# Kernel tuning notes

Measured on AMD Instinct MI355X. Metric: run time of the kernel, lower is better.

The kernel has to match this reference:

```python
import jax, jax.numpy as jnp
import numpy as np

N_NODES = 100000


def gcn_conv(x, edge_index, W, b):
    """PyG-style GCNConv: self-loops + symmetric norm + scatter-add aggregation."""
    n = x.shape[0]
    loop = jnp.arange(n, dtype=edge_index.dtype)
    src = jnp.concatenate([edge_index[0], loop])  # [E+N]
    dst = jnp.concatenate([edge_index[1], loop])  # [E+N]
    # degree of target nodes (edge weight = 1)
    deg = jax.ops.segment_sum(jnp.ones_like(dst, dtype=x.dtype), dst, num_segments=n)
    dinv = jnp.where(deg > 0, jax.lax.rsqrt(deg), 0.0)
    norm = dinv[src] * dinv[dst]  # [E+N]
    h = x @ W                      # [N, out] linear (bias added post-aggregation)
    msg = h[src] * norm[:, None]   # [E+N, out]
    out = jax.ops.segment_sum(msg, dst, num_segments=n)
    return out + b


def setup_inputs() -> dict:
    key = jax.random.key(0)
    ks = jax.random.split(key, 8)
    n, e = N_NODES, 3200000
    x = jax.random.normal(ks[0], (n, 11), dtype=jnp.float32)
    edge_index = jax.random.randint(ks[1], (2, e), 0, n, dtype=jnp.int32)
    def glorot(k, fi, fo):
        s = jnp.sqrt(6.0 / (fi + fo))
        return jax.random.uniform(k, (fi, fo), dtype=jnp.float32, minval=-s, maxval=s)
    return {
        "x": x,
        "edge_index": edge_index,
        "W1": glorot(ks[2], 11, 16), "b1": jnp.zeros((16,), jnp.float32),
        "W2": glorot(ks[3], 16, 32), "b2": jnp.zeros((32,), jnp.float32),
        "W3": glorot(ks[4], 32, 64), "b3": jnp.zeros((64,), jnp.float32),
    }


def reference(x, edge_index, W1, b1, W2, b2, W3, b3):
    # dropout is identity in eval mode
    h = jax.nn.relu(gcn_conv(x, edge_index, W1, b1))
    h = jax.nn.relu(gcn_conv(h, edge_index, W2, b2))
    return gcn_conv(h, edge_index, W3, b3)
```

## Files before the change

### kernel.cpp

```cpp
#include <hip/hip_runtime.h>
#include <hip/hip_fp16.h>

#define NPB_SHIFT 7
#define NPB       128
#define CHUNK     8192
#define STAGE_CAP 8192
#define NBKT_MAX  1024

union U2H { unsigned u; __half2 h; };

__device__ inline float2 h2f(unsigned u) {
    U2H c; c.u = u;
    return __half22float2(c.h);
}

__device__ inline unsigned f2h(float a, float b) {
    U2H c; c.h = __float22half2_rn(make_float2(a, b));
    return c.u;
}


__global__ void hist_kernel(const int* __restrict__ dst, int* __restrict__ hist,
                            int E, int HBr, int nbkt) {
    __shared__ int bins[NBKT_MAX];
    int tid = threadIdx.x;
    for (int i = tid; i < nbkt; i += 512) bins[i] = 0;
    __syncthreads();
    int start = blockIdx.x * CHUNK;
    #pragma unroll
    for (int j = 0; j < 16; ++j) {
        int e = start + j * 512 + tid;
        if (e < E) atomicAdd(&bins[dst[e] >> NPB_SHIFT], 1);
    }
    __syncthreads();
    for (int i = tid; i < nbkt; i += 512)
        hist[(size_t)i * HBr + blockIdx.x] = bins[i];
}


__global__ void scan_block8_kernel(int* data, int* __restrict__ partial, int len) {
    __shared__ int wtot[16];
    int tid = threadIdx.x, lane = tid & 63, wid = tid >> 6;
    int base = blockIdx.x * 8192 + tid * 8;
    int v[8]; int s = 0;
    #pragma unroll
    for (int j = 0; j < 8; ++j) {
        int i = base + j;
        v[j] = (i < len) ? data[i] : 0;
        s += v[j];
    }
    int inc = s;
    #pragma unroll
    for (int o = 1; o < 64; o <<= 1) { int t = __shfl_up(inc, o); if (lane >= o) inc += t; }
    if (lane == 63) wtot[wid] = inc;
    __syncthreads();
    if (tid == 0) {
        int run = 0;
        #pragma unroll
        for (int w = 0; w < 16; ++w) { int t = wtot[w]; wtot[w] = run; run += t; }
        partial[blockIdx.x] = run;
    }
    __syncthreads();
    int excl = wtot[wid] + inc - s;
    #pragma unroll
    for (int j = 0; j < 8; ++j) {
        int i = base + j;
        if (i < len) data[i] = excl;
        excl += v[j];
    }
}

__global__ void scan_partials_kernel(int* partial, int nb) {
    int t = threadIdx.x;
    int i0 = 2 * t, i1 = 2 * t + 1;
    int v0 = (i0 < nb) ? partial[i0] : 0;
    int v1 = (i1 < nb) ? partial[i1] : 0;
    int s = v0 + v1;
    int inc = s;
    #pragma unroll
    for (int o = 1; o < 64; o <<= 1) { int u = __shfl_up(inc, o); if (t >= o) inc += u; }
    int excl = inc - s;
    if (i0 < nb) partial[i0] = excl;
    if (i1 < nb) partial[i1] = excl + v0;
}


__global__ void scatter_kernel(const int* __restrict__ src, const int* __restrict__ dst,
                               const int* __restrict__ offbuf, const int* __restrict__ partial,
                               int* __restrict__ ebuf, int E, int HBr, int nbkt) {
    __shared__ int gbase[NBKT_MAX];
    __shared__ int thist[NBKT_MAX];
    __shared__ int toff[NBKT_MAX + 1];
    __shared__ int stage[CHUNK];
    __shared__ unsigned short bstage[CHUNK];
    __shared__ int wtot8[8];
    int tid = threadIdx.x, lane = tid & 63, wid = tid >> 6;
    for (int i = tid; i < nbkt; i += 512) {
        size_t idx = (size_t)i * HBr + blockIdx.x;
        gbase[i] = offbuf[idx] + partial[(int)(idx >> 13)];
    }
    for (int i = tid; i < NBKT_MAX; i += 512) thist[i] = 0;
    __syncthreads();
    int start = blockIdx.x * CHUNK;
    int s_[16], d_[16], r_[16];
    #pragma unroll
    for (int j = 0; j < 16; ++j) {
        int e = start + j * 512 + tid;
        if (e < E) {
            s_[j] = src[e];
            d_[j] = dst[e];
            r_[j] = atomicAdd(&thist[d_[j] >> NPB_SHIFT], 1);
        } else {
            d_[j] = -1;
        }
    }
    __syncthreads();
    int a0 = thist[2 * tid], a1 = thist[2 * tid + 1];
    int ss = a0 + a1;
    int inc = ss;
    #pragma unroll
    for (int o = 1; o < 64; o <<= 1) { int t = __shfl_up(inc, o); if (lane >= o) inc += t; }
    if (lane == 63) wtot8[wid] = inc;
    __syncthreads();
    int wbase = 0;
    for (int w = 0; w < wid; ++w) wbase += wtot8[w];
    int excl = wbase + inc - ss;
    toff[2 * tid]     = excl;
    toff[2 * tid + 1] = excl + a0;
    if (tid == 511) toff[1024] = excl + ss;
    __syncthreads();
    #pragma unroll
    for (int j = 0; j < 16; ++j) {
        if (d_[j] >= 0) {
            int b = d_[j] >> NPB_SHIFT;
            int q = toff[b] + r_[j];
            stage[q]  = ((d_[j] & (NPB - 1)) << 17) | s_[j];
            bstage[q] = (unsigned short)b;
        }
    }
    __syncthreads();
    int total = toff[1024];
    for (int j = tid; j < total; j += 512) {
        int b = bstage[j];
        ebuf[gbase[b] + (j - toff[b])] = stage[j];
    }
}


__global__ void bucket_build_kernel(const int* __restrict__ ebuf, const int* __restrict__ offbuf,
                                    const int* __restrict__ partial, const float* __restrict__ x,
                                    int* __restrict__ csr_src, int* __restrict__ row_start,
                                    float* __restrict__ dinv, unsigned* __restrict__ g0h,
                                    int E, int HBr, int nbkt, int n) {
    __shared__ int cnt[NPB], cur[NPB];
    __shared__ float dnl[NPB];
    __shared__ int stage[STAGE_CAP];
    __shared__ int wtot2[2];
    int tid = threadIdx.x;
    int k = blockIdx.x;
    size_t ib = (size_t)k * HBr;
    int bb = offbuf[ib] + partial[(int)(ib >> 13)];
    int be;
    if (k + 1 < nbkt) {
        size_t ie = (size_t)(k + 1) * HBr;
        be = offbuf[ie] + partial[(int)(ie >> 13)];
    } else be = E;
    int bsize = be - bb;
    if (tid < NPB) cnt[tid] = 0;
    __syncthreads();

    constexpr int J = 20;
    int v[J], r[J];
    bool fast = (bsize <= J * 256) && (bsize <= STAGE_CAP);
    if (fast) {
        #pragma unroll
        for (int j = 0; j < J; ++j) {
            int e = bb + tid + j * 256;
            if (e < be) { v[j] = ebuf[e]; r[j] = atomicAdd(&cnt[v[j] >> 17], 1); }
            else v[j] = -1;
        }
    } else {
        for (int e = bb + tid; e < be; e += 256) atomicAdd(&cnt[ebuf[e] >> 17], 1);
    }
    __syncthreads();

    int lane = tid & 63, wid = tid >> 6;
    int c = 0, inc = 0;
    if (tid < NPB) {
        c = cnt[tid];
        inc = c;
        #pragma unroll
        for (int o = 1; o < 64; o <<= 1) { int t = __shfl_up(inc, o); if (lane >= o) inc += t; }
        if (lane == 63) wtot2[wid] = inc;
    }
    __syncthreads();
    if (tid < NPB) {
        int base = (wid == 1) ? wtot2[0] : 0;
        int excl = base + inc - c;
        cur[tid] = excl;
        int node = k * NPB + tid;
        if (node < n) {
            row_start[node] = bb + excl;
            float dn = rsqrtf((float)(c + 1));
            dinv[node] = dn;
            dnl[tid] = dn;
        }
    }
    if (k == 0 && tid == 0) row_start[n] = E;
    __syncthreads();

    {
        int base_node = k * NPB;
        for (int i = tid; i < NPB * 8; i += 256) {
            int ln = i >> 3, kk = i & 7;
            int node = base_node + ln;
            if (node < n) {
                float dn = dnl[ln];
                int f0 = 2 * kk, f1 = f0 + 1;
                float a = (f0 < 11) ? x[(size_t)node * 11 + f0] * dn : 0.f;
                float b = (f1 < 11) ? x[(size_t)node * 11 + f1] * dn : 0.f;
                g0h[(size_t)node * 8 + kk] = f2h(a, b);
            }
        }
    }

    if (fast) {
        #pragma unroll
        for (int j = 0; j < J; ++j)
            if (v[j] >= 0) stage[cur[v[j] >> 17] + r[j]] = v[j] & 0x1FFFF;
        __syncthreads();
        for (int j = tid; j < bsize; j += 256) csr_src[bb + j] = stage[j];
    } else if (bsize <= STAGE_CAP) {
        for (int e = bb + tid; e < be; e += 256) {
            int vv = ebuf[e];
            int rr = atomicAdd(&cur[vv >> 17], 1);
            stage[rr] = vv & 0x1FFFF;
        }
        __syncthreads();
        for (int j = tid; j < bsize; j += 256) csr_src[bb + j] = stage[j];
    } else {
        for (int e = bb + tid; e < be; e += 256) {
            int vv = ebuf[e];
            int rr = atomicAdd(&cur[vv >> 17], 1);
            csr_src[bb + rr] = vv & 0x1FFFF;
        }
    }
}


template <int LPR, int NB>
__device__ inline void gather_batch_h(const uint2* __restrict__ gv, const int* __restrict__ csr,
                                      int p, int end, int nrem, int q, int grp, float* acc) {
    constexpr int NGRP = 16 / LPR;
    int s[NB]; float m[NB];
    #pragma unroll
    for (int u = 0; u < NB; ++u) {
        int slot = u * NGRP + grp;
        s[u] = csr[min(p + slot, end - 1)];
        m[u] = (slot < nrem) ? 1.f : 0.f;
    }
    uint2 v[NB];
    #pragma unroll
    for (int u = 0; u < NB; ++u) v[u] = gv[(size_t)s[u] * LPR + q];
    #pragma unroll
    for (int u = 0; u < NB; ++u) {
        float2 a = h2f(v[u].x), b = h2f(v[u].y);
        acc[0] = fmaf(m[u], a.x, acc[0]);
        acc[1] = fmaf(m[u], a.y, acc[1]);
        acc[2] = fmaf(m[u], b.x, acc[2]);
        acc[3] = fmaf(m[u], b.y, acc[3]);
    }
}

template <int FIN>
__global__ void aggregate_kernel(const uint2* __restrict__ gv,
                                 const int* __restrict__ row_start,
                                 const int* __restrict__ csr_src,
                                 const float* __restrict__ dinv,
                                 float4* __restrict__ pre, int n) {
    constexpr int LPR  = FIN / 4;
    constexpr int NGRP = 16 / LPR;
    int lane  = threadIdx.x & 63;
    int wid   = threadIdx.x >> 6;
    int sub   = lane >> 4;
    int slane = lane & 15;
    int node  = (blockIdx.x * (blockDim.x >> 6) + wid) * 4 + sub;
    if (node >= n) return;
    int q   = slane & (LPR - 1);
    int grp = slane / LPR;
    int beg = row_start[node];
    int end = row_start[node + 1];
    float acc[4] = {0.f, 0.f, 0.f, 0.f};

    int p = beg;
    for (; p + 8 * NGRP <= end; p += 8 * NGRP) {
        int s[8];
        #pragma unroll
        for (int u = 0; u < 8; ++u) s[u] = csr_src[p + u * NGRP + grp];
        uint2 v[8];
        #pragma unroll
        for (int u = 0; u < 8; ++u) v[u] = gv[(size_t)s[u] * LPR + q];
        #pragma unroll
        for (int u = 0; u < 8; ++u) {
            float2 a = h2f(v[u].x), b = h2f(v[u].y);
            acc[0] += a.x; acc[1] += a.y; acc[2] += b.x; acc[3] += b.y;
        }
    }
    int nrem = end - p;
    if (nrem > 0) {
        if (nrem <= NGRP)          gather_batch_h<LPR, 1>(gv, csr_src, p, end, nrem, q, grp, acc);
        else if (nrem <= 2 * NGRP) gather_batch_h<LPR, 2>(gv, csr_src, p, end, nrem, q, grp, acc);
        else if (nrem <= 4 * NGRP) gather_batch_h<LPR, 4>(gv, csr_src, p, end, nrem, q, grp, acc);
        else                       gather_batch_h<LPR, 8>(gv, csr_src, p, end, nrem, q, grp, acc);
    }

    #pragma unroll
    for (int off = LPR; off < 16; off <<= 1)
        #pragma unroll
        for (int c = 0; c < 4; ++c) acc[c] += __shfl_xor(acc[c], off);

    float dn = dinv[node];
    uint2 sv = gv[(size_t)node * LPR + q];
    float2 a = h2f(sv.x), b = h2f(sv.y);
    float4 o;
    o.x = dn * (acc[0] + a.x);
    o.y = dn * (acc[1] + a.y);
    o.z = dn * (acc[2] + b.x);
    o.w = dn * (acc[3] + b.y);
    if (grp == 0) pre[(size_t)node * LPR + q] = o;
}


template <int FINP, int FINR, int FOUT, bool RELU, bool SCALE, bool HALFOUT>
__global__ void linear_kernel(const float* __restrict__ pre, const float* __restrict__ W,
                              const float* __restrict__ bias, const float* __restrict__ dinv,
                              void* __restrict__ outv, int n) {
    __shared__ float sW[FINP * FOUT];
    __shared__ float sB[FOUT];
    for (int i = threadIdx.x; i < FINP * FOUT; i += blockDim.x)
        sW[i] = (i < FINR * FOUT) ? W[i] : 0.f;
    for (int i = threadIdx.x; i < FOUT; i += blockDim.x) sB[i] = bias[i];
    __syncthreads();
    int node = blockIdx.x * blockDim.x + threadIdx.x;
    if (node >= n) return;
    float xi[FINP];
    #pragma unroll
    for (int k = 0; k < FINP; ++k) xi[k] = pre[(size_t)node * FINP + k];
    float s = SCALE ? dinv[node] : 1.f;
    float o[FOUT];
    #pragma unroll
    for (int fo = 0; fo < FOUT; ++fo) {
        float acc = sB[fo];
        #pragma unroll
        for (int k = 0; k < FINP; ++k) acc = fmaf(xi[k], sW[k * FOUT + fo], acc);
        if (RELU) acc = fmaxf(acc, 0.f);
        o[fo] = acc * s;
    }
    if constexpr (HALFOUT) {
        unsigned* outh = (unsigned*)outv;
        #pragma unroll
        for (int fo = 0; fo < FOUT / 2; ++fo)
            outh[(size_t)node * (FOUT / 2) + fo] = f2h(o[2 * fo], o[2 * fo + 1]);
    } else {
        float* outf = (float*)outv;
        #pragma unroll
        for (int fo = 0; fo < FOUT; ++fo) outf[(size_t)node * FOUT + fo] = o[fo];
    }
}


extern "C" void kernel_launch(void* const* d_in, const int* in_sizes, int n_in,
                              void* d_out, int out_size, void* d_ws, size_t ws_size,
                              hipStream_t stream) {
    const float* x  = (const float*)d_in[0];
    const int*   ei = (const int*)d_in[1];
    const float* W1 = (const float*)d_in[2];
    const float* b1 = (const float*)d_in[3];
    const float* W2 = (const float*)d_in[4];
    const float* b2 = (const float*)d_in[5];
    const float* W3 = (const float*)d_in[6];
    const float* b3 = (const float*)d_in[7];
    float* out = (float*)d_out;

    const int n = in_sizes[0] / 11;
    const int E = in_sizes[1] / 2;
    const int* src = ei;
    const int* dst = ei + E;

    const int nbkt = (n + NPB - 1) >> NPB_SHIFT;
    const int HBr  = (E + CHUNK - 1) / CHUNK;
    const size_t len = (size_t)nbkt * HBr;
    const int nb = (int)((len + 8191) / 8192);

    char* ws = (char*)d_ws;
    size_t off = 0;
    auto alloc = [&](size_t bytes) {
        void* p = ws + off;
        off = (off + bytes + 255) & ~(size_t)255;
        return p;
    };
    int*      offbuf    = (int*)     alloc(len * 4);
    int*      partial   = (int*)     alloc((size_t)128 * 4);
    int*      ebuf      = (int*)     alloc((size_t)E * 4);
    int*      csr_src   = (int*)     alloc((size_t)E * 4);
    int*      row_start = (int*)     alloc((size_t)(n + 1) * 4);
    float*    dinv      = (float*)   alloc((size_t)n * 4);
    unsigned* g0h       = (unsigned*)alloc((size_t)n * 16 * 2);
    unsigned* g1h       = (unsigned*)alloc((size_t)n * 16 * 2);
    unsigned* g2h       = (unsigned*)alloc((size_t)n * 32 * 2);
    float*    preS      = (float*)   alloc((size_t)n * 16 * 4);
    float*    preL      = (float*)   alloc((size_t)n * 32 * 4);
    (void)ws_size;

    const int B = 256;
    int gn   = (n + B - 1) / B;
    int gagg = (n + 15) / 16;

    hist_kernel<<<HBr, 512, 0, stream>>>(dst, offbuf, E, HBr, nbkt);
    scan_block8_kernel<<<nb, 1024, 0, stream>>>(offbuf, partial, (int)len);
    scan_partials_kernel<<<1, 64, 0, stream>>>(partial, nb);
    scatter_kernel<<<HBr, 512, 0, stream>>>(src, dst, offbuf, partial, ebuf, E, HBr, nbkt);
    bucket_build_kernel<<<nbkt, 256, 0, stream>>>(ebuf, offbuf, partial, x, csr_src, row_start,
                                                  dinv, g0h, E, HBr, nbkt, n);

    aggregate_kernel<16><<<gagg, B, 0, stream>>>((const uint2*)g0h, row_start, csr_src, dinv,
                                                 (float4*)preS, n);
    linear_kernel<16, 11, 16, true, true, true><<<gn, B, 0, stream>>>(preS, W1, b1, dinv, g1h, n);

    aggregate_kernel<16><<<gagg, B, 0, stream>>>((const uint2*)g1h, row_start, csr_src, dinv,
                                                 (float4*)preS, n);
    linear_kernel<16, 16, 32, true, true, true><<<gn, B, 0, stream>>>(preS, W2, b2, dinv, g2h, n);

    aggregate_kernel<32><<<gagg, B, 0, stream>>>((const uint2*)g2h, row_start, csr_src, dinv,
                                                 (float4*)preL, n);
    linear_kernel<32, 32, 64, false, false, false><<<gn, B, 0, stream>>>(preL, W3, b3, dinv, out, n);
}
```

Measured before the change: 176.9 us.

## Split layer-3 features into two half-width tables and fold partial scan into consumers

The layer-2 linear output is written as two separate 16-feature half-precision tables, and the third aggregation runs as two 16-wide passes that write interleaved halves of the fp32 pre-activation buffer. Each gathered row is then 32 bytes instead of 64, so each random-access working set is smaller and may stay cache-resident, at the cost of walking the CSR index array twice. Separately, the single-block scan of partial sums is removed and recomputed redundantly in each scatter and bucket-build block, saving one tiny launch but adding a small per-block wave scan.

Result: slower. 189.0 us (+6.8%).

```diff
diff --git a/kernel.cpp b/kernel.cpp
--- a/kernel.cpp
+++ b/kernel.cpp
@@ -70,24 +70,11 @@
     }
 }
 
-__global__ void scan_partials_kernel(int* partial, int nb) {
-    int t = threadIdx.x;
-    int i0 = 2 * t, i1 = 2 * t + 1;
-    int v0 = (i0 < nb) ? partial[i0] : 0;
-    int v1 = (i1 < nb) ? partial[i1] : 0;
-    int s = v0 + v1;
-    int inc = s;
-    #pragma unroll
-    for (int o = 1; o < 64; o <<= 1) { int u = __shfl_up(inc, o); if (t >= o) inc += u; }
-    int excl = inc - s;
-    if (i0 < nb) partial[i0] = excl;
-    if (i1 < nb) partial[i1] = excl + v0;
-}
-
 
 __global__ void scatter_kernel(const int* __restrict__ src, const int* __restrict__ dst,
                                const int* __restrict__ offbuf, const int* __restrict__ partial,
-                               int* __restrict__ ebuf, int E, int HBr, int nbkt) {
+                               int* __restrict__ ebuf, int E, int HBr, int nbkt, int nbp) {
+    __shared__ int psum[64];
     __shared__ int gbase[NBKT_MAX];
     __shared__ int thist[NBKT_MAX];
     __shared__ int toff[NBKT_MAX + 1];
@@ -95,12 +82,19 @@
     __shared__ unsigned short bstage[CHUNK];
     __shared__ int wtot8[8];
     int tid = threadIdx.x, lane = tid & 63, wid = tid >> 6;
+    if (tid < 64) {
+        int v = (tid < nbp) ? partial[tid] : 0;
+        int inc = v;
+        #pragma unroll
+        for (int o = 1; o < 64; o <<= 1) { int t = __shfl_up(inc, o); if (tid >= o) inc += t; }
+        psum[tid] = inc - v;
+    }
+    for (int i = tid; i < NBKT_MAX; i += 512) thist[i] = 0;
+    __syncthreads();
     for (int i = tid; i < nbkt; i += 512) {
         size_t idx = (size_t)i * HBr + blockIdx.x;
-        gbase[i] = offbuf[idx] + partial[(int)(idx >> 13)];
-    }
-    for (int i = tid; i < NBKT_MAX; i += 512) thist[i] = 0;
-    __syncthreads();
+        gbase[i] = offbuf[idx] + psum[(int)(idx >> 13)];
+    }
     int start = blockIdx.x * CHUNK;
     int s_[16], d_[16], r_[16];
     #pragma unroll
@@ -151,23 +145,32 @@
                                     const int* __restrict__ partial, const float* __restrict__ x,
                                     int* __restrict__ csr_src, int* __restrict__ row_start,
                                     float* __restrict__ dinv, unsigned* __restrict__ g0h,
-                                    int E, int HBr, int nbkt, int n) {
+                                    int E, int HBr, int nbkt, int n, int nbp) {
+    __shared__ int psum[64];
     __shared__ int cnt[NPB], cur[NPB];
     __shared__ float dnl[NPB];
     __shared__ int stage[STAGE_CAP];
     __shared__ int wtot2[2];
     int tid = threadIdx.x;
     int k = blockIdx.x;
+    if (tid < 64) {
+        int v = (tid < nbp) ? partial[tid] : 0;
+        int inc = v;
+        #pragma unroll
+        for (int o = 1; o < 64; o <<= 1) { int t = __shfl_up(inc, o); if (tid >= o) inc += t; }
+        psum[tid] = inc - v;
+    }
+    if (tid < NPB) cnt[tid] = 0;
+    __syncthreads();
+
     size_t ib = (size_t)k * HBr;
-    int bb = offbuf[ib] + partial[(int)(ib >> 13)];
+    int bb = offbuf[ib] + psum[(int)(ib >> 13)];
     int be;
     if (k + 1 < nbkt) {
         size_t ie = (size_t)(k + 1) * HBr;
-        be = offbuf[ie] + partial[(int)(ie >> 13)];
+        be = offbuf[ie] + psum[(int)(ie >> 13)];
     } else be = E;
     int bsize = be - bb;
-    if (tid < NPB) cnt[tid] = 0;
-    __syncthreads();
 
     constexpr int J = 20;
     int v[J], r[J];
@@ -277,7 +280,7 @@
                                  const int* __restrict__ row_start,
                                  const int* __restrict__ csr_src,
                                  const float* __restrict__ dinv,
-                                 float4* __restrict__ pre, int n) {
+                                 float4* __restrict__ pre, int n, int s4, int off4) {
     constexpr int LPR  = FIN / 4;
     constexpr int NGRP = 16 / LPR;
     int lane  = threadIdx.x & 63;
@@ -327,14 +330,14 @@
     o.y = dn * (acc[1] + a.y);
     o.z = dn * (acc[2] + b.x);
     o.w = dn * (acc[3] + b.y);
-    if (grp == 0) pre[(size_t)node * LPR + q] = o;
-}
-
-
-template <int FINP, int FINR, int FOUT, bool RELU, bool SCALE, bool HALFOUT>
+    if (grp == 0) pre[(size_t)node * s4 + off4 + q] = o;
+}
+
+
+template <int FINP, int FINR, int FOUT, bool RELU, bool SCALE, bool HALFOUT, bool SPLIT>
 __global__ void linear_kernel(const float* __restrict__ pre, const float* __restrict__ W,
                               const float* __restrict__ bias, const float* __restrict__ dinv,
-                              void* __restrict__ outv, int n) {
+                              void* __restrict__ outv, void* __restrict__ outv2, int n) {
     __shared__ float sW[FINP * FOUT];
     __shared__ float sB[FOUT];
     for (int i = threadIdx.x; i < FINP * FOUT; i += blockDim.x)
@@ -357,10 +360,21 @@
         o[fo] = acc * s;
     }
     if constexpr (HALFOUT) {
-        unsigned* outh = (unsigned*)outv;
-        #pragma unroll
-        for (int fo = 0; fo < FOUT / 2; ++fo)
-            outh[(size_t)node * (FOUT / 2) + fo] = f2h(o[2 * fo], o[2 * fo + 1]);
+        if constexpr (SPLIT) {
+            unsigned* oa = (unsigned*)outv;
+            unsigned* ob = (unsigned*)outv2;
+            #pragma unroll
+            for (int fo = 0; fo < FOUT / 2; fo += 2)
+                oa[(size_t)node * (FOUT / 4) + (fo >> 1)] = f2h(o[fo], o[fo + 1]);
+            #pragma unroll
+            for (int fo = FOUT / 2; fo < FOUT; fo += 2)
+                ob[(size_t)node * (FOUT / 4) + ((fo - FOUT / 2) >> 1)] = f2h(o[fo], o[fo + 1]);
+        } else {
+            unsigned* outh = (unsigned*)outv;
+            #pragma unroll
+            for (int fo = 0; fo < FOUT / 2; ++fo)
+                outh[(size_t)node * (FOUT / 2) + fo] = f2h(o[2 * fo], o[2 * fo + 1]);
+        }
     } else {
         float* outf = (float*)outv;
         #pragma unroll
@@ -407,7 +421,8 @@
     float*    dinv      = (float*)   alloc((size_t)n * 4);
     unsigned* g0h       = (unsigned*)alloc((size_t)n * 16 * 2);
     unsigned* g1h       = (unsigned*)alloc((size_t)n * 16 * 2);
-    unsigned* g2h       = (unsigned*)alloc((size_t)n * 32 * 2);
+    unsigned* g2a       = (unsigned*)alloc((size_t)n * 16 * 2);
+    unsigned* g2b       = (unsigned*)alloc((size_t)n * 16 * 2);
     float*    preS      = (float*)   alloc((size_t)n * 16 * 4);
     float*    preL      = (float*)   alloc((size_t)n * 32 * 4);
     (void)ws_size;
@@ -418,20 +433,24 @@
 
     hist_kernel<<<HBr, 512, 0, stream>>>(dst, offbuf, E, HBr, nbkt);
     scan_block8_kernel<<<nb, 1024, 0, stream>>>(offbuf, partial, (int)len);
-    scan_partials_kernel<<<1, 64, 0, stream>>>(partial, nb);
-    scatter_kernel<<<HBr, 512, 0, stream>>>(src, dst, offbuf, partial, ebuf, E, HBr, nbkt);
+    scatter_kernel<<<HBr, 512, 0, stream>>>(src, dst, offbuf, partial, ebuf, E, HBr, nbkt, nb);
     bucket_build_kernel<<<nbkt, 256, 0, stream>>>(ebuf, offbuf, partial, x, csr_src, row_start,
-                                                  dinv, g0h, E, HBr, nbkt, n);
+                                                  dinv, g0h, E, HBr, nbkt, n, nb);
 
     aggregate_kernel<16><<<gagg, B, 0, stream>>>((const uint2*)g0h, row_start, csr_src, dinv,
-                                                 (float4*)preS, n);
-    linear_kernel<16, 11, 16, true, true, true><<<gn, B, 0, stream>>>(preS, W1, b1, dinv, g1h, n);
+                                                 (float4*)preS, n, 4, 0);
+    linear_kernel<16, 11, 16, true, true, true, false>
+        <<<gn, B, 0, stream>>>(preS, W1, b1, dinv, g1h, nullptr, n);
 
     aggregate_kernel<16><<<gagg, B, 0, stream>>>((const uint2*)g1h, row_start, csr_src, dinv,
-                                                 (float4*)preS, n);
-    linear_kernel<16, 16, 32, true, true, true><<<gn, B, 0, stream>>>(preS, W2, b2, dinv, g2h, n);
-
-    aggregate_kernel<32><<<gagg, B, 0, stream>>>((const uint2*)g2h, row_start, csr_src, dinv,
-                                                 (float4*)preL, n);
-    linear_kernel<32, 32, 64, false, false, false><<<gn, B, 0, stream>>>(preL, W3, b3, dinv, out, n);
-}
+                                                 (float4*)preS, n, 4, 0);
+    linear_kernel<16, 16, 32, true, true, true, true>
+        <<<gn, B, 0, stream>>>(preS, W2, b2, dinv, g2a, g2b, n);
+
+    aggregate_kernel<16><<<gagg, B, 0, stream>>>((const uint2*)g2a, row_start, csr_src, dinv,
+                                                 (float4*)preL, n, 8, 0);
+    aggregate_kernel<16><<<gagg, B, 0, stream>>>((const uint2*)g2b, row_start, csr_src, dinv,
+                                                 (float4*)preL, n, 8, 4);
+    linear_kernel<32, 32, 64, false, false, false, false>
+        <<<gn, B, 0, stream>>>(preL, W3, b3, dinv, out, nullptr, n);
+}
```
